# Kernel tuning notes

Measured on AMD Instinct MI355X. Metric: run time of the kernel, lower is better.

Reference implementation:

```python
import jax, jax.numpy as jnp
import numpy as np

NEG = -1e9
TAU = 1.0
N_SAMPLES = 5
SWEEP = (0.1, 0.5, 5)


def layer_norm(x, g, b, eps=1e-5):
    m = x.mean(-1, keepdims=True)
    v = x.var(-1, keepdims=True)
    return (x - m) / jnp.sqrt(v + eps) * g + b


def entmax15(z):
    # exact 1.5-entmax along last axis (Peters & Martins 2019 sort-based algorithm)
    z = z / 2.0
    zs = jnp.sort(z, axis=-1)[..., ::-1]               # descending
    T = z.shape[-1]
    kk = jnp.arange(1, T + 1, dtype=z.dtype)
    mean = jnp.cumsum(zs, -1) / kk
    mean_sq = jnp.cumsum(zs * zs, -1) / kk
    ss = kk * (mean_sq - mean * mean)
    delta = jnp.clip((1.0 - ss) / kk, 0.0)
    tau = mean - jnp.sqrt(delta)
    support = jnp.sum((tau <= zs).astype(jnp.int32), -1, keepdims=True)  # k_star
    tau_star = jnp.take_along_axis(tau, support - 1, axis=-1)
    return jnp.square(jnp.clip(z - tau_star, 0.0))


def stochastic_topk(key, scores, attn, k, tau, n_samples):
    # vectorized over samples AND batch rows with per-row variable k:
    # threshold = k-th largest perturbed score per row (ties measure-zero w/ gumbel)
    u = jax.random.uniform(key, (n_samples,) + scores.shape)
    noise = -jnp.log(-jnp.log(u + 1e-6) + 1e-6)
    pert = jnp.where(attn[None] == 0, NEG, scores[None] + noise * tau)  # [S,B,T]
    srt = jnp.sort(pert, -1)[..., ::-1]
    idx = jnp.broadcast_to((k - 1)[None, :, None], pert.shape[:2] + (1,))
    thr = jnp.take_along_axis(srt, idx, axis=-1)       # [S,B,1]
    h = (pert >= thr).astype(scores.dtype)
    return h.mean(0)                                   # [B,T]


def pool(tok, attn):
    # masked mean pooling (stand-in for sent_encoder.pool)
    return (tok * attn[..., None]).sum(1) / jnp.clip(attn.sum(1, keepdims=True), 1e-6)


def _forward(ids, embeddings, attn, ln_g, ln_b, W1, b1, W2, b2, emb_table):
    emb = embeddings * attn[..., None]
    h = jax.nn.gelu(layer_norm(emb, ln_g, ln_b) @ W1 + b1, approximate=False)
    scores = (h @ W2 + b2)[..., 0]                     # [B,T]
    scores = jnp.where(attn == 0, NEG, scores)

    tok = emb_table[ids]                               # stand-in token embeddings
    full_rep = jax.lax.stop_gradient(pool(tok, attn))  # torch.no_grad path

    T_eff = attn.sum(1)                                # [B]
    # g_soft is identical across the rho sweep in the original; hoisted here
    g_soft = entmax15(scores / TAU) * attn
    g_soft = g_soft / jnp.clip(g_soft.sum(1, keepdims=True), 1e-6)

    key = jax.random.key(42)
    rhos = np.linspace(*SWEEP)
    g_sweep, loss_sweep, rho_eff_sweep = [], [], []
    recon_sum = jnp.zeros((), embeddings.dtype)
    g = None
    for j, rho in enumerate(rhos):
        k = jnp.maximum((float(rho) * T_eff).astype(jnp.int32), 1)
        g_hard = stochastic_topk(jax.random.fold_in(key, j), scores, attn, k, TAU, N_SAMPLES)
        # straight-through: hard forward, soft (entmax) backward
        g = jax.lax.stop_gradient(g_hard) - jax.lax.stop_gradient(g_soft) + g_soft
        rho_eff_sweep.append(g.sum(1) / T_eff)
        eff_attn = attn * g
        pred_rep = pool(tok, eff_attn)
        l_r = jnp.mean(jnp.square(pred_rep - full_rep))  # recon_loss = MSE stand-in
        recon_sum = recon_sum + l_r
        g_sweep.append(g)
        loss_sweep.append(l_r)
    recon_avg = recon_sum / len(rhos)
    return g, jnp.stack(g_sweep), recon_avg, jnp.stack(loss_sweep), jnp.stack(rho_eff_sweep)


def setup_inputs() -> dict:
    key = jax.random.key(0)
    B, T, D, H, V = 8, 2048, 1024, 1365, 32000
    ks = jax.random.split(key, 8)
    return {
        "ids": jax.random.randint(ks[0], (B, T), 0, V),
        "embeddings": jax.random.normal(ks[1], (B, T, D), jnp.float32),
        "attn": jnp.ones((B, T), jnp.float32),
        "ln_g": jnp.ones((D,), jnp.float32),
        "ln_b": jnp.zeros((D,), jnp.float32),
        "W1": jax.random.normal(ks[2], (D, H), jnp.float32) * 0.02,
        "b1": jnp.zeros((H,), jnp.float32),
        "W2": jax.random.normal(ks[3], (H, 1), jnp.float32) * 0.02,
        "b2": jnp.zeros((1,), jnp.float32),
        "emb_table": jax.random.normal(ks[4], (V, D), jnp.float32) * 0.02,
    }


def reference(ids, embeddings, attn, ln_g, ln_b, W1, b1, W2, b2, emb_table):
    return _forward(ids, embeddings, attn, ln_g, ln_b, W1, b1, W2, b2, emb_table)
```

## Files before the change

### kernel.cpp

```cpp
#include <hip/hip_runtime.h>
#include <math.h>
#include <stdint.h>

#define B_ 8
#define T_ 2048
#define D_ 1024
#define H_ 1365
#define HPAD 1536
#define NTOK (B_*T_)
#define NSAMP 5
#define NRHO 5

typedef float  f32x4  __attribute__((ext_vector_type(4)));
typedef __bf16 bf16x8 __attribute__((ext_vector_type(8)));

#define WS_SCORES 0
#define WS_CNT    (WS_SCORES + NTOK*8)
#define WS_PREDW  (WS_CNT + NRHO*B_*T_*4)
#define WS_FULLW  (WS_PREDW + NRHO*B_*D_*8)
#define WS_SUMEFF (WS_FULLW + B_*D_*8)
#define WS_SUMATT (WS_SUMEFF + NRHO*B_*8)
#define WS_SUMG   (WS_SUMATT + B_*8)
#define WS_LR     (WS_SUMG + NRHO*B_*8)
#define WS_ZERO_BYTES (WS_LR + NRHO*8)
#define WS_STATS  WS_ZERO_BYTES
#define WS_W1THI  (WS_STATS + NTOK*8)
#define WS_W1TLO  (WS_W1THI + (size_t)HPAD*D_*2)
#define WS_AHI    (WS_W1TLO + (size_t)HPAD*D_*2)
#define WS_ALO    (WS_AHI + (size_t)NTOK*D_*2)
#define WS_FULL_END (WS_ALO + (size_t)NTOK*D_*2)

#define OUT_G      0
#define OUT_GSW    16384
#define OUT_RECON  98304
#define OUT_LOSS   98305
#define OUT_RHOEFF 98310

__device__ inline unsigned short f2bf(float x) {
    uint32_t u = __float_as_uint(x);
    return (unsigned short)((u + 0x7FFFu + ((u >> 16) & 1u)) >> 16);
}

__launch_bounds__(256)
__global__ void k_w1t(const float* __restrict__ W1, unsigned short* __restrict__ hi,
                      unsigned short* __restrict__ lo)
{
    __shared__ float tile[32][33];
    const int tid = threadIdx.x;
    const int bk = blockIdx.x & 31;
    const int bh = blockIdx.x >> 5;
    const int k0 = bk * 32, h0 = bh * 32;
    const int a = tid & 31, b = tid >> 5;
    #pragma unroll
    for (int i = 0; i < 4; ++i) {
        int k = k0 + b + i * 8;
        int h = h0 + a;
        tile[b + i*8][a] = (h < H_) ? W1[(size_t)k * H_ + h] : 0.0f;
    }
    __syncthreads();
    #pragma unroll
    for (int i = 0; i < 4; ++i) {
        int hrow = h0 + b + i * 8;
        int kcol = k0 + a;
        float v = tile[a][b + i*8];
        unsigned short hb = f2bf(v);
        float hf = __uint_as_float((uint32_t)hb << 16);
        unsigned short lb = f2bf(v - hf);
        size_t dst = (size_t)hrow * D_ + kcol;
        hi[dst] = hb; lo[dst] = lb;
    }
}

__launch_bounds__(256)
__global__ void k_asplit(const float* __restrict__ emb, const float* __restrict__ attn,
                         const float* __restrict__ ln_g, const float* __restrict__ ln_b,
                         unsigned short* __restrict__ ahi, unsigned short* __restrict__ alo)
{
    const int tid = threadIdx.x, l = tid & 63, w = tid >> 6;
    const int t0 = blockIdx.x * 64;
    for (int tk = w; tk < 64; tk += 4) {
        const int tg = t0 + tk;
        const float av = attn[tg];
        const float* row = emb + (size_t)tg * D_;
        float rv[16];
        double s1 = 0.0, s2 = 0.0;
        #pragma unroll
        for (int i = 0; i < 16; ++i) {
            rv[i] = row[i*64 + l];
            double x = (double)rv[i] * (double)av;
            s1 += x; s2 += x * x;
        }
        for (int m = 32; m; m >>= 1) { s1 += __shfl_xor(s1, m); s2 += __shfl_xor(s2, m); }
        double mean = s1 / (double)D_;
        double var  = s2 / (double)D_ - mean * mean;
        double inv  = 1.0 / sqrt(var + 1e-5);
        float sc  = (float)((double)av * inv);
        float nsh = -(float)(mean * inv);
        #pragma unroll
        for (int i = 0; i < 16; ++i) {
            int k = i * 64 + l;
            float t  = fmaf(rv[i], sc, nsh);
            float xn = fmaf(t, ln_g[k], ln_b[k]);
            unsigned short hb = f2bf(xn);
            float hf = __uint_as_float((uint32_t)hb << 16);
            size_t dst = (size_t)tg * D_ + k;
            ahi[dst] = hb;
            alo[dst] = f2bf(xn - hf);
        }
    }
}

__launch_bounds__(256)
__global__ void k_stats(const float* __restrict__ emb, const float* __restrict__ attn,
                        float2* __restrict__ stats)
{
    const int tid = threadIdx.x, l = tid & 63, w = tid >> 6;
    const int t0 = blockIdx.x * 64;
    for (int tk = w; tk < 64; tk += 4) {
        const int tg = t0 + tk;
        const float av = attn[tg];
        const float* row = emb + (size_t)tg * D_;
        double s1 = 0.0, s2 = 0.0;
        #pragma unroll
        for (int i = 0; i < D_/64; ++i) {
            double x = (double)row[i*64 + l] * (double)av;
            s1 += x; s2 += x * x;
        }
        for (int m = 32; m; m >>= 1) { s1 += __shfl_xor(s1, m); s2 += __shfl_xor(s2, m); }
        if (l == 0) {
            double mean = s1 / (double)D_;
            double var  = s2 / (double)D_ - mean * mean;
            double inv  = 1.0 / sqrt(var + 1e-5);
            stats[tg] = make_float2((float)((double)av * inv), (float)(mean * inv));
        }
    }
}

#define ABUF_U 8192
#define KSTEPS 32

__device__ __forceinline__ void gll16(const unsigned short* g, unsigned short* l)
{
    __builtin_amdgcn_global_load_lds((const __attribute__((address_space(1))) void*)g,
                                     (__attribute__((address_space(3))) void*)l, 16, 0, 0);
}

__launch_bounds__(512, 2)
__global__ void k_scores8(const unsigned short* __restrict__ ahi,
                          const unsigned short* __restrict__ alo,
                          const unsigned short* __restrict__ w1thi,
                          const unsigned short* __restrict__ w1tlo,
                          const float* __restrict__ b1, const float* __restrict__ W2,
                          double* __restrict__ scores)
{
    __shared__ __align__(16) unsigned short smem[3*ABUF_U];

    const int tid = threadIdx.x;
    const int blk = blockIdx.x;
    const int lin = (blk & 7) * 96 + (blk >> 3);
    const int hh = lin >> 7, mm = lin & 127;
    const int t0 = mm * 128;
    const int h0 = hh * 256;

    const int l  = tid & 63, w = tid >> 6;
    const int wr = w >> 2, wcn = w & 3;
    const int lm = l & 15, lq = l >> 4;

    const int lrow  = l >> 2;
    const int lslot = (l & 3) ^ ((l >> 3) & 3);
    const unsigned short* sA_hi = ahi + (size_t)(t0 + w*16 + lrow) * D_ + lslot*8;
    const unsigned short* sA_lo = alo + (size_t)(t0 + w*16 + lrow) * D_ + lslot*8;
    const int dA = w*512;

    const int sw8 = (lq ^ ((lm >> 1) & 3)) * 8;
    int offA[4];
    #pragma unroll
    for (int r = 0; r < 4; ++r) offA[r] = (wr*64 + r*16 + lm)*32 + sw8;

    const unsigned short* bBh = w1thi + (size_t)(h0 + wcn*64 + lm) * D_ + lq*8;
    const unsigned short* bBl = w1tlo + (size_t)(h0 + wcn*64 + lm) * D_ + lq*8;

    f32x4 acc[4][4];
    #pragma unroll
    for (int r = 0; r < 4; ++r)
        #pragma unroll
        for (int c = 0; c < 4; ++c) acc[r][c] = (f32x4){0.f, 0.f, 0.f, 0.f};

    bf16x8 bhp[2][4], blp[2][4];
    gll16(sA_hi,      &smem[0*ABUF_U + dA]);
    gll16(sA_lo,      &smem[0*ABUF_U + dA + 4096]);
    gll16(sA_hi + 32, &smem[1*ABUF_U + dA]);
    gll16(sA_lo + 32, &smem[1*ABUF_U + dA + 4096]);
    #pragma unroll
    for (int c = 0; c < 4; ++c) {
        bhp[0][c] = *(const bf16x8*)&bBh[(size_t)c*16*D_];
        blp[0][c] = *(const bf16x8*)&bBl[(size_t)c*16*D_];
    }
    #pragma unroll
    for (int c = 0; c < 4; ++c) {
        bhp[1][c] = *(const bf16x8*)&bBh[(size_t)c*16*D_ + 32];
        blp[1][c] = *(const bf16x8*)&bBl[(size_t)c*16*D_ + 32];
    }
    asm volatile("s_waitcnt vmcnt(8)" ::: "memory");
    asm volatile("s_barrier" ::: "memory");

    #pragma unroll
    for (int t = 0; t < KSTEPS; ++t) {
        const int cur = t & 1;
        bf16x8 ah[4], al[4];
        const int ab = (t % 3) * ABUF_U;
        #pragma unroll
        for (int r = 0; r < 4; ++r) ah[r] = *(const bf16x8*)&smem[ab + offA[r]];
        #pragma unroll
        for (int r = 0; r < 4; ++r) al[r] = *(const bf16x8*)&smem[ab + 4096 + offA[r]];
        if (t + 2 < KSTEPS) {
            const int ab2 = ((t + 2) % 3) * ABUF_U;
            gll16(sA_hi + (t+2)*32, &smem[ab2 + dA]);
            gll16(sA_lo + (t+2)*32, &smem[ab2 + dA + 4096]);
        }
        __builtin_amdgcn_s_setprio(1);
        #pragma unroll
        for (int r = 0; r < 4; ++r)
            #pragma unroll
            for (int c = 0; c < 4; ++c)
                acc[r][c] = __builtin_amdgcn_mfma_f32_16x16x32_bf16(ah[r], bhp[cur][c], acc[r][c], 0, 0, 0);
        #pragma unroll
        for (int r = 0; r < 4; ++r)
            #pragma unroll
            for (int c = 0; c < 4; ++c)
                acc[r][c] = __builtin_amdgcn_mfma_f32_16x16x32_bf16(ah[r], blp[cur][c], acc[r][c], 0, 0, 0);
        #pragma unroll
        for (int r = 0; r < 4; ++r)
            #pragma unroll
            for (int c = 0; c < 4; ++c)
                acc[r][c] = __builtin_amdgcn_mfma_f32_16x16x32_bf16(al[r], bhp[cur][c], acc[r][c], 0, 0, 0);
        __builtin_amdgcn_s_setprio(0);
        if (t + 2 < KSTEPS) {
            #pragma unroll
            for (int c = 0; c < 4; ++c) {
                bhp[cur][c] = *(const bf16x8*)&bBh[(size_t)c*16*D_ + (t+2)*32];
                blp[cur][c] = *(const bf16x8*)&bBl[(size_t)c*16*D_ + (t+2)*32];
            }
        }
        if (t < KSTEPS - 2)       asm volatile("s_waitcnt vmcnt(10)" ::: "memory");
        else if (t == KSTEPS - 2) asm volatile("s_waitcnt vmcnt(0)" ::: "memory");
        if (t < KSTEPS - 1)       asm volatile("s_barrier" ::: "memory");
    }

    float b1v[4], w2v[4];
    #pragma unroll
    for (int c = 0; c < 4; ++c) {
        int hg = h0 + wcn*64 + c*16 + lm;
        bool ok = (hg < H_);
        b1v[c] = ok ? b1[hg] : 0.0f;
        w2v[c] = ok ? W2[hg] : 0.0f;
    }
    const float is2 = 0.70710678118654752440f;
    #pragma unroll
    for (int r = 0; r < 4; ++r) {
        #pragma unroll
        for (int i = 0; i < 4; ++i) {
            float ps = 0.0f;
            #pragma unroll
            for (int c = 0; c < 4; ++c) {
                float z  = acc[r][c][i] + b1v[c];
                float gl = 0.5f * z * (1.0f + erff(z * is2));
                ps = fmaf(gl, w2v[c], ps);
            }
            double psd = (double)ps;
            psd += __shfl_xor(psd, 1);
            psd += __shfl_xor(psd, 2);
            psd += __shfl_xor(psd, 4);
            psd += __shfl_xor(psd, 8);
            if (lm == 0)
                atomicAdd(&scores[t0 + wr*64 + r*16 + lq*4 + i], psd);
        }
    }
}

__launch_bounds__(256)
__global__ void k_scores_fb(const float* __restrict__ emb, const float* __restrict__ ln_g,
                            const float* __restrict__ ln_b, const float2* __restrict__ stats,
                            const unsigned short* __restrict__ w1thi,
                            const unsigned short* __restrict__ w1tlo,
                            const float* __restrict__ b1, const float* __restrict__ W2,
                            double* __restrict__ scores)
{
    __shared__ __align__(16) unsigned short sAhi[128*40];
    __shared__ __align__(16) unsigned short sAlo[128*40];
    __shared__ __align__(16) unsigned short sBhi[128*40];
    __shared__ __align__(16) unsigned short sBlo[128*40];
    __shared__ float sS1[128], sS2[128];

    const int tid = threadIdx.x;
    const int blk = blockIdx.x;
    const int xcd = blk & 7, slot = blk >> 3;
    const int lin = xcd * 176 + slot;
    const int tt = lin / 11, hh = lin - tt * 11;
    const int t0 = tt * 128;
    const int h0 = hh * 128;

    if (tid < 128) {
        float2 st = stats[t0 + tid];
        sS1[tid] = st.x; sS2[tid] = st.y;
    }
    f32x4 acc[4][4];
    #pragma unroll
    for (int r = 0; r < 4; ++r)
        #pragma unroll
        for (int c = 0; c < 4; ++c) acc[r][c] = (f32x4){0.f, 0.f, 0.f, 0.f};
    const int l = tid & 63, w = tid >> 6;
    const int lm = l & 15, lq = l >> 4;
    const int wr = (w >> 1) * 64;
    const int wc = (w & 1) * 64;
    __syncthreads();

    for (int kc = 0; kc < D_; kc += 32) {
        #pragma unroll
        for (int r2 = 0; r2 < 2; ++r2) {
            int g = tid + r2 * 256;
            int row = g >> 2, oct = g & 3;
            size_t src = (size_t)(h0 + row) * D_ + kc + oct * 8;
            int dst = row * 40 + oct * 8;
            *(bf16x8*)&sBhi[dst] = *(const bf16x8*)&w1thi[src];
            *(bf16x8*)&sBlo[dst] = *(const bf16x8*)&w1tlo[src];
        }
        #pragma unroll
        for (int r2 = 0; r2 < 2; ++r2) {
            int g = tid + r2 * 256;
            int tk = g >> 2, oct = g & 3;
            int tg = t0 + tk, dg = kc + oct * 8;
            const float* ep = emb + (size_t)tg * D_ + dg;
            float s1 = sS1[tk], ns2 = -sS2[tk];
            union { unsigned short s[8]; bf16x8 v; } hi, lo;
            #pragma unroll
            for (int j = 0; j < 8; ++j) {
                float t  = fmaf(ep[j], s1, ns2);
                float xn = fmaf(t, ln_g[dg + j], ln_b[dg + j]);
                unsigned short hb = f2bf(xn);
                float hf = __uint_as_float((uint32_t)hb << 16);
                hi.s[j] = hb;
                lo.s[j] = f2bf(xn - hf);
            }
            int dst = tk * 40 + oct * 8;
            *(bf16x8*)&sAhi[dst] = hi.v;
            *(bf16x8*)&sAlo[dst] = lo.v;
        }
        __syncthreads();
        bf16x8 ah[4], al[4], bh[4], bl[4];
        #pragma unroll
        for (int r = 0; r < 4; ++r) {
            int off = (wr + r * 16 + lm) * 40 + lq * 8;
            ah[r] = *(const bf16x8*)&sAhi[off];
            al[r] = *(const bf16x8*)&sAlo[off];
        }
        #pragma unroll
        for (int c = 0; c < 4; ++c) {
            int off = (wc + c * 16 + lm) * 40 + lq * 8;
            bh[c] = *(const bf16x8*)&sBhi[off];
            bl[c] = *(const bf16x8*)&sBlo[off];
        }
        #pragma unroll
        for (int r = 0; r < 4; ++r)
            #pragma unroll
            for (int c = 0; c < 4; ++c) {
                acc[r][c] = __builtin_amdgcn_mfma_f32_16x16x32_bf16(ah[r], bh[c], acc[r][c], 0, 0, 0);
                acc[r][c] = __builtin_amdgcn_mfma_f32_16x16x32_bf16(ah[r], bl[c], acc[r][c], 0, 0, 0);
                acc[r][c] = __builtin_amdgcn_mfma_f32_16x16x32_bf16(al[r], bh[c], acc[r][c], 0, 0, 0);
            }
        __syncthreads();
    }
    float b1v[4], w2v[4];
    #pragma unroll
    for (int c = 0; c < 4; ++c) {
        int hg = h0 + wc + c * 16 + lm;
        bool ok = (hg < H_);
        b1v[c] = ok ? b1[hg] : 0.0f;
        w2v[c] = ok ? W2[hg] : 0.0f;
    }
    const float is2 = 0.70710678118654752440f;
    #pragma unroll
    for (int r = 0; r < 4; ++r) {
        #pragma unroll
        for (int i = 0; i < 4; ++i) {
            float ps = 0.0f;
            #pragma unroll
            for (int c = 0; c < 4; ++c) {
                float z  = acc[r][c][i] + b1v[c];
                float gl = 0.5f * z * (1.0f + erff(z * is2));
                ps = fmaf(gl, w2v[c], ps);
            }
            double psd = (double)ps;
            psd += __shfl_xor(psd, 1);
            psd += __shfl_xor(psd, 2);
            psd += __shfl_xor(psd, 4);
            psd += __shfl_xor(psd, 8);
            if (lm == 0)
                atomicAdd(&scores[t0 + wr + r * 16 + lq * 4 + i], psd);
        }
    }
}

__device__ inline void tf2x32(uint32_t k0, uint32_t k1, uint32_t x0, uint32_t x1,
                              uint32_t& o0, uint32_t& o1)
{
    const uint32_t ks2 = k0 ^ k1 ^ 0x1BD11BDAu;
    x0 += k0; x1 += k1;
#define ROT_(v,d) (((v) << (d)) | ((v) >> (32 - (d))))
#define RND_(R) { x0 += x1; x1 = ROT_(x1, R); x1 ^= x0; }
    RND_(13) RND_(15) RND_(26) RND_(6)
    x0 += k1;  x1 += ks2 + 1u;
    RND_(17) RND_(29) RND_(16) RND_(24)
    x0 += ks2; x1 += k0 + 2u;
    RND_(13) RND_(15) RND_(26) RND_(6)
    x0 += k0;  x1 += k1 + 3u;
    RND_(17) RND_(29) RND_(16) RND_(24)
    x0 += k1;  x1 += ks2 + 4u;
    RND_(13) RND_(15) RND_(26) RND_(6)
    x0 += ks2; x1 += k0 + 5u;
    o0 = x0; o1 = x1;
#undef RND_
#undef ROT_
}

__launch_bounds__(256)
__global__ void k_topk(const double* __restrict__ scores, const float* __restrict__ attn,
                       const float* __restrict__ b2, int* __restrict__ cnt)
{
    __shared__ unsigned long long keys[2048];
    __shared__ unsigned int hist[256];
    __shared__ unsigned int wsum[4];
    __shared__ unsigned int selDigit, selBase;
    __shared__ double red[4];

    const int tid = threadIdx.x;
    const int blk = blockIdx.x;
    const int j = blk / 40;
    const int s = (blk % 40) >> 3;
    const int b = blk & 7;

    uint32_t kk0, kk1;
    tf2x32(0u, 42u, 0u, (uint32_t)j, kk0, kk1);

    double tsum = 0.0;
    for (int t = tid; t < T_; t += 256) tsum += (double)attn[b * T_ + t];
    for (int m = 32; m; m >>= 1) tsum += __shfl_xor(tsum, m);
    if ((tid & 63) == 0) red[tid >> 6] = tsum;
    __syncthreads();
    const double Teff = red[0] + red[1] + red[2] + red[3];
    const float rhos[5] = {0.1f, 0.2f, 0.3f, 0.4f, 0.5f};
    int kst = (int)(rhos[j] * (float)Teff);
    if (kst < 1) kst = 1;

    const double bb2 = (double)b2[0];
    #pragma unroll
    for (int r = 0; r < 8; ++r) {
        int t = tid + r * 256;
        int f = (s * 8 + b) * T_ + t;
        uint32_t o0, o1;
        tf2x32(kk0, kk1, 0u, (uint32_t)f, o0, o1);
        uint32_t bits = o0 ^ o1;
        float u = __uint_as_float((bits >> 9) | 0x3f800000u) - 1.0f;
        float a1 = (float)((double)u + (double)1e-6f);
        float la = (float)log((double)a1);
        float m1 = (float)((double)1e-6f - (double)la);
        float lb = (float)log((double)m1);
        float noise = -lb;
        float av = attn[b * T_ + t];
        double pv = (av == 0.0f) ? -1e9 : (scores[b * T_ + t] + bb2 + (double)noise);
        unsigned long long uu = (unsigned long long)__double_as_longlong(pv);
        keys[t] = (uu >> 63) ? ~uu : (uu | 0x8000000000000000ull);
    }
    __syncthreads();

    unsigned long long pfx = 0;
    unsigned int plo = (unsigned int)(2048 - kst);
    const int lane = tid & 63, wv = tid >> 6;
    for (int pass = 0; pass < 8; ++pass) {
        const int shift = 56 - 8 * pass;
        const unsigned long long maskhi = (pass == 0) ? 0ull : (~0ull << (64 - 8 * pass));
        hist[tid] = 0;
        __syncthreads();
        #pragma unroll
        for (int r = 0; r < 8; ++r) {
            unsigned long long kk = keys[tid + r * 256];
            if ((kk & maskhi) == pfx)
                atomicAdd(&hist[(unsigned int)((kk >> shift) & 255ull)], 1u);
        }
        __syncthreads();
        unsigned int own = hist[tid];
        int val = (int)own;
        #pragma unroll
        for (int off = 1; off < 64; off <<= 1) {
            int n = __shfl_up(val, off);
            if (lane >= off) val += n;
        }
        if (lane == 63) wsum[wv] = (unsigned int)val;
        __syncthreads();
        unsigned int woff = 0;
        for (int q = 0; q < wv; ++q) woff += wsum[q];
        unsigned int incl = (unsigned int)val + woff;
        unsigned int excl = incl - own;
        if (own > 0 && plo >= excl && plo < incl) { selDigit = (unsigned int)tid; selBase = excl; }
        __syncthreads();
        pfx |= ((unsigned long long)selDigit << shift);
        plo -= selBase;
        __syncthreads();
    }

    #pragma unroll
    for (int r = 0; r < 8; ++r) {
        int t = tid + r * 256;
        if (keys[t] >= pfx) atomicAdd(&cnt[(j * 8 + b) * T_ + t], 1);
    }
}

__launch_bounds__(256)
__global__ void k_gfin(const int* __restrict__ cnt, const float* __restrict__ attn,
                       float* __restrict__ out, double* __restrict__ sumeff,
                       double* __restrict__ sumatt, double* __restrict__ sumg)
{
    __shared__ double redA[4], redB[4], redC[4];
    const int j = blockIdx.x >> 3, b = blockIdx.x & 7;
    const int tid = threadIdx.x;
    double sg = 0.0, se = 0.0, sa = 0.0;
    for (int t = tid; t < T_; t += 256) {
        int c = cnt[(j * 8 + b) * T_ + t];
        float g  = (float)c / 5.0f;
        float av = attn[b * T_ + t];
        out[OUT_GSW + (j * 8 + b) * T_ + t] = g;
        if (j == 4) out[OUT_G + b * T_ + t] = g;
        sg += (double)g;
        se += (double)(av * g);
        sa += (double)av;
    }
    for (int m = 32; m; m >>= 1) { sg += __shfl_xor(sg, m); se += __shfl_xor(se, m); sa += __shfl_xor(sa, m); }
    if ((tid & 63) == 0) { redA[tid>>6] = sg; redB[tid>>6] = se; redC[tid>>6] = sa; }
    __syncthreads();
    if (tid == 0) {
        sg = redA[0]+redA[1]+redA[2]+redA[3];
        se = redB[0]+redB[1]+redB[2]+redB[3];
        sa = redC[0]+redC[1]+redC[2]+redC[3];
        sumg[j*8+b] = sg; sumeff[j*8+b] = se;
        if (j == 0) sumatt[b] = sa;
        out[OUT_RHOEFF + j*8 + b] = (float)sg / (float)sa;
    }
}

__launch_bounds__(256)
__global__ void k_pool(const int* __restrict__ ids, const float* __restrict__ attn,
                       const float* __restrict__ out, const float* __restrict__ emb_table,
                       double* __restrict__ predw, double* __restrict__ fullw)
{
    __shared__ int   sid[128];
    __shared__ float sw[6][128];
    const int blk = blockIdx.x;
    const int b  = blk >> 6;
    const int dc = (blk >> 4) & 3;
    const int tc = blk & 15;
    const int tid = threadIdx.x;
    const int d = dc * 256 + tid;
    if (tid < 128) {
        int t = tc * 128 + tid;
        sid[tid] = ids[b * T_ + t];
        float av = attn[b * T_ + t];
        sw[0][tid] = av;
        #pragma unroll
        for (int j = 0; j < 5; ++j) {
            float g = out[OUT_GSW + (j * 8 + b) * T_ + t];
            sw[1 + j][tid] = av * g;
        }
    }
    __syncthreads();
    double acc[6] = {0,0,0,0,0,0};
    #pragma unroll 4
    for (int i = 0; i < 128; ++i) {
        float val = emb_table[(size_t)sid[i] * D_ + d];
        #pragma unroll
        for (int c = 0; c < 6; ++c) acc[c] += (double)(val * sw[c][i]);
    }
    atomicAdd(&fullw[b * D_ + d], acc[0]);
    #pragma unroll
    for (int j = 0; j < 5; ++j)
        atomicAdd(&predw[(j * 8 + b) * D_ + d], acc[1 + j]);
}

__launch_bounds__(256)
__global__ void k_loss(const double* __restrict__ predw, const double* __restrict__ fullw,
                       const double* __restrict__ sumeff, const double* __restrict__ sumatt,
                       float* __restrict__ out, double* __restrict__ lrws)
{
    __shared__ double red[4];
    const int j = blockIdx.x;
    const int tid = threadIdx.x;
    double p = 0.0;
    for (int i = tid; i < B_ * D_; i += 256) {
        int b = i >> 10;
        double dF = sumatt[b];        if (dF < 1e-6) dF = 1e-6;
        double dE = sumeff[j*8 + b];  if (dE < 1e-6) dE = 1e-6;
        double diff = predw[j * B_ * D_ + i] / dE - fullw[i] / dF;
        p += diff * diff;
    }
    for (int m = 32; m; m >>= 1) p += __shfl_xor(p, m);
    if ((tid & 63) == 0) red[tid >> 6] = p;
    __syncthreads();
    if (tid == 0) {
        double t = red[0] + red[1] + red[2] + red[3];
        float lr = (float)(t / (double)(B_ * D_));
        out[OUT_LOSS + j] = lr;
        lrws[j] = (double)lr;
    }
}

__launch_bounds__(64)
__global__ void k_lfin(const double* __restrict__ lrws, float* __restrict__ out)
{
    if (threadIdx.x == 0) {
        float srec = 0.0f;
        for (int j = 0; j < 5; ++j) srec += (float)lrws[j];
        out[OUT_RECON] = srec / 5.0f;
    }
}

extern "C" void kernel_launch(void* const* d_in, const int* in_sizes, int n_in,
                              void* d_out, int out_size, void* d_ws, size_t ws_size,
                              hipStream_t stream)
{
    const int*   ids  = (const int*)  d_in[0];
    const float* emb  = (const float*)d_in[1];
    const float* attn = (const float*)d_in[2];
    const float* ln_g = (const float*)d_in[3];
    const float* ln_b = (const float*)d_in[4];
    const float* W1   = (const float*)d_in[5];
    const float* b1   = (const float*)d_in[6];
    const float* W2   = (const float*)d_in[7];
    const float* b2   = (const float*)d_in[8];
    const float* et   = (const float*)d_in[9];
    float* out = (float*)d_out;
    char*  ws  = (char*)d_ws;

    double* scores = (double*)(ws + WS_SCORES);
    int*    cnt    = (int*)   (ws + WS_CNT);
    double* predw  = (double*)(ws + WS_PREDW);
    double* fullw  = (double*)(ws + WS_FULLW);
    double* sumeff = (double*)(ws + WS_SUMEFF);
    double* sumatt = (double*)(ws + WS_SUMATT);
    double* sumg   = (double*)(ws + WS_SUMG);
    double* lrws   = (double*)(ws + WS_LR);
    float2* stats  = (float2*)(ws + WS_STATS);
    unsigned short* w1thi = (unsigned short*)(ws + WS_W1THI);
    unsigned short* w1tlo = (unsigned short*)(ws + WS_W1TLO);
    unsigned short* ahi   = (unsigned short*)(ws + WS_AHI);
    unsigned short* alo   = (unsigned short*)(ws + WS_ALO);

    hipMemsetAsync(d_ws, 0, WS_ZERO_BYTES, stream);

    k_w1t<<<48*32, 256, 0, stream>>>(W1, w1thi, w1tlo);
    if (ws_size >= WS_FULL_END) {
        k_asplit<<<NTOK/64, 256, 0, stream>>>(emb, attn, ln_g, ln_b, ahi, alo);
        k_scores8<<<768, 512, 0, stream>>>(ahi, alo, w1thi, w1tlo, b1, W2, scores);
    } else {
        k_stats<<<NTOK/64, 256, 0, stream>>>(emb, attn, stats);
        k_scores_fb<<<1408, 256, 0, stream>>>(emb, ln_g, ln_b, stats, w1thi, w1tlo,
                                              b1, W2, scores);
    }
    k_topk<<<NRHO * NSAMP * B_, 256, 0, stream>>>(scores, attn, b2, cnt);
    k_gfin<<<NRHO * B_, 256, 0, stream>>>(cnt, attn, out, sumeff, sumatt, sumg);
    k_pool<<<512, 256, 0, stream>>>(ids, attn, out, et, predw, fullw);
    k_loss<<<NRHO, 256, 0, stream>>>(predw, fullw, sumeff, sumatt, out, lrws);
    k_lfin<<<1, 64, 0, stream>>>(lrws, out);
}
```

Before: 575.6 us.

## Stage W1 tiles through LDS and prefetch LDS fragments one step ahead

The B operand (W1 hi/lo transposed) is now loaded into LDS with global_load_lds alongside A, instead of each wave reading it directly from global memory into registers. A/B fragments for the next k-step are read from LDS into registers while the current step's MFMAs run, and the block-to-tile mapping changes so that consecutive blocks share a token tile across the six H tiles. The goal is to cut redundant global traffic for W1 and improve L2 reuse of A. In exchange LDS use triples to 144KB per block, which likely limits occupancy to one block per CU despite the launch bounds of two, and each step now waits on vmcnt(0) before its barrier.

```diff
diff --git a/kernel.cpp b/kernel.cpp
--- a/kernel.cpp
+++ b/kernel.cpp
@@ -136,7 +136,7 @@
     }
 }
 
-#define ABUF_U 8192
+#define BUF_U 24576
 #define KSTEPS 32
 
 __device__ __forceinline__ void gll16(const unsigned short* g, unsigned short* l)
@@ -153,12 +153,12 @@
                           const float* __restrict__ b1, const float* __restrict__ W2,
                           double* __restrict__ scores)
 {
-    __shared__ __align__(16) unsigned short smem[3*ABUF_U];
+    __shared__ __align__(16) unsigned short smem[3*BUF_U];
 
     const int tid = threadIdx.x;
     const int blk = blockIdx.x;
     const int lin = (blk & 7) * 96 + (blk >> 3);
-    const int hh = lin >> 7, mm = lin & 127;
+    const int mm = lin / 6, hh = lin - mm * 6;
     const int t0 = mm * 128;
     const int h0 = hh * 256;
 
@@ -168,17 +168,22 @@
 
     const int lrow  = l >> 2;
     const int lslot = (l & 3) ^ ((l >> 3) & 3);
-    const unsigned short* sA_hi = ahi + (size_t)(t0 + w*16 + lrow) * D_ + lslot*8;
-    const unsigned short* sA_lo = alo + (size_t)(t0 + w*16 + lrow) * D_ + lslot*8;
-    const int dA = w*512;
+    const unsigned short* sA_hi  = ahi   + (size_t)(t0 + w*16 + lrow) * D_ + lslot*8;
+    const unsigned short* sA_lo  = alo   + (size_t)(t0 + w*16 + lrow) * D_ + lslot*8;
+    const unsigned short* sB_hi0 = w1thi + (size_t)(h0 + w*32 + lrow) * D_ + lslot*8;
+    const unsigned short* sB_hi1 = sB_hi0 + 16*D_;
+    const unsigned short* sB_lo0 = w1tlo + (size_t)(h0 + w*32 + lrow) * D_ + lslot*8;
+    const unsigned short* sB_lo1 = sB_lo0 + 16*D_;
+    const int dAhi  = w*512,           dAlo  = 4096 + w*512;
+    const int dBhi0 = 8192 + w*1024,   dBhi1 = dBhi0 + 512;
+    const int dBlo0 = 16384 + w*1024,  dBlo1 = dBlo0 + 512;
 
     const int sw8 = (lq ^ ((lm >> 1) & 3)) * 8;
-    int offA[4];
+    int offA[4], offB[4];
     #pragma unroll
     for (int r = 0; r < 4; ++r) offA[r] = (wr*64 + r*16 + lm)*32 + sw8;
-
-    const unsigned short* bBh = w1thi + (size_t)(h0 + wcn*64 + lm) * D_ + lq*8;
-    const unsigned short* bBl = w1tlo + (size_t)(h0 + wcn*64 + lm) * D_ + lq*8;
+    #pragma unroll
+    for (int c = 0; c < 4; ++c) offB[c] = 8192 + (wcn*64 + c*16 + lm)*32 + sw8;
 
     f32x4 acc[4][4];
     #pragma unroll
@@ -186,65 +191,76 @@
         #pragma unroll
         for (int c = 0; c < 4; ++c) acc[r][c] = (f32x4){0.f, 0.f, 0.f, 0.f};
 
-    bf16x8 bhp[2][4], blp[2][4];
-    gll16(sA_hi,      &smem[0*ABUF_U + dA]);
-    gll16(sA_lo,      &smem[0*ABUF_U + dA + 4096]);
-    gll16(sA_hi + 32, &smem[1*ABUF_U + dA]);
-    gll16(sA_lo + 32, &smem[1*ABUF_U + dA + 4096]);
-    #pragma unroll
-    for (int c = 0; c < 4; ++c) {
-        bhp[0][c] = *(const bf16x8*)&bBh[(size_t)c*16*D_];
-        blp[0][c] = *(const bf16x8*)&bBl[(size_t)c*16*D_];
-    }
-    #pragma unroll
-    for (int c = 0; c < 4; ++c) {
-        bhp[1][c] = *(const bf16x8*)&bBh[(size_t)c*16*D_ + 32];
-        blp[1][c] = *(const bf16x8*)&bBl[(size_t)c*16*D_ + 32];
-    }
-    asm volatile("s_waitcnt vmcnt(8)" ::: "memory");
+    gll16(sA_hi,       &smem[0*BUF_U + dAhi]);
+    gll16(sA_lo,       &smem[0*BUF_U + dAlo]);
+    gll16(sB_hi0,      &smem[0*BUF_U + dBhi0]);
+    gll16(sB_hi1,      &smem[0*BUF_U + dBhi1]);
+    gll16(sB_lo0,      &smem[0*BUF_U + dBlo0]);
+    gll16(sB_lo1,      &smem[0*BUF_U + dBlo1]);
+    gll16(sA_hi  + 32, &smem[1*BUF_U + dAhi]);
+    gll16(sA_lo  + 32, &smem[1*BUF_U + dAlo]);
+    gll16(sB_hi0 + 32, &smem[1*BUF_U + dBhi0]);
+    gll16(sB_hi1 + 32, &smem[1*BUF_U + dBhi1]);
+    gll16(sB_lo0 + 32, &smem[1*BUF_U + dBlo0]);
+    gll16(sB_lo1 + 32, &smem[1*BUF_U + dBlo1]);
+    asm volatile("s_waitcnt vmcnt(6)" ::: "memory");
     asm volatile("s_barrier" ::: "memory");
 
+    bf16x8 ahp[2][4], alp[2][4], bhp[2][4];
+    #pragma unroll
+    for (int r = 0; r < 4; ++r) {
+        ahp[0][r] = *(const bf16x8*)&smem[offA[r]];
+        alp[0][r] = *(const bf16x8*)&smem[offA[r] + 4096];
+    }
+    #pragma unroll
+    for (int c = 0; c < 4; ++c) bhp[0][c] = *(const bf16x8*)&smem[offB[c]];
+
     #pragma unroll
     for (int t = 0; t < KSTEPS; ++t) {
-        const int cur = t & 1;
-        bf16x8 ah[4], al[4];
-        const int ab = (t % 3) * ABUF_U;
-        #pragma unroll
-        for (int r = 0; r < 4; ++r) ah[r] = *(const bf16x8*)&smem[ab + offA[r]];
-        #pragma unroll
-        for (int r = 0; r < 4; ++r) al[r] = *(const bf16x8*)&smem[ab + 4096 + offA[r]];
+        const int cur = t & 1, nxt = cur ^ 1;
+        asm volatile("s_waitcnt vmcnt(0)" ::: "memory");
+        asm volatile("s_barrier" ::: "memory");
         if (t + 2 < KSTEPS) {
-            const int ab2 = ((t + 2) % 3) * ABUF_U;
-            gll16(sA_hi + (t+2)*32, &smem[ab2 + dA]);
-            gll16(sA_lo + (t+2)*32, &smem[ab2 + dA + 4096]);
+            const int eb = ((t + 2) % 3) * BUF_U;
+            const int ko = (t + 2) * 32;
+            gll16(sA_hi  + ko, &smem[eb + dAhi]);
+            gll16(sA_lo  + ko, &smem[eb + dAlo]);
+            gll16(sB_hi0 + ko, &smem[eb + dBhi0]);
+            gll16(sB_hi1 + ko, &smem[eb + dBhi1]);
+            gll16(sB_lo0 + ko, &smem[eb + dBlo0]);
+            gll16(sB_lo1 + ko, &smem[eb + dBlo1]);
+        }
+        bf16x8 bl[4];
+        const int db = (t % 3) * BUF_U;
+        #pragma unroll
+        for (int c = 0; c < 4; ++c) bl[c] = *(const bf16x8*)&smem[db + offB[c] + 8192];
+        if (t + 1 < KSTEPS) {
+            const int nb = ((t + 1) % 3) * BUF_U;
+            #pragma unroll
+            for (int r = 0; r < 4; ++r) {
+                ahp[nxt][r] = *(const bf16x8*)&smem[nb + offA[r]];
+                alp[nxt][r] = *(const bf16x8*)&smem[nb + offA[r] + 4096];
+            }
+            #pragma unroll
+            for (int c = 0; c < 4; ++c) bhp[nxt][c] = *(const bf16x8*)&smem[nb + offB[c]];
         }
         __builtin_amdgcn_s_setprio(1);
         #pragma unroll
         for (int r = 0; r < 4; ++r)
             #pragma unroll
             for (int c = 0; c < 4; ++c)
-                acc[r][c] = __builtin_amdgcn_mfma_f32_16x16x32_bf16(ah[r], bhp[cur][c], acc[r][c], 0, 0, 0);
+                acc[r][c] = __builtin_amdgcn_mfma_f32_16x16x32_bf16(ahp[cur][r], bhp[cur][c], acc[r][c], 0, 0, 0);
         #pragma unroll
         for (int r = 0; r < 4; ++r)
             #pragma unroll
             for (int c = 0; c < 4; ++c)
-                acc[r][c] = __builtin_amdgcn_mfma_f32_16x16x32_bf16(ah[r], blp[cur][c], acc[r][c], 0, 0, 0);
+                acc[r][c] = __builtin_amdgcn_mfma_f32_16x16x32_bf16(ahp[cur][r], bl[c], acc[r][c], 0, 0, 0);
         #pragma unroll
         for (int r = 0; r < 4; ++r)
             #pragma unroll
             for (int c = 0; c < 4; ++c)
-                acc[r][c] = __builtin_amdgcn_mfma_f32_16x16x32_bf16(al[r], bhp[cur][c], acc[r][c], 0, 0, 0);
+                acc[r][c] = __builtin_amdgcn_mfma_f32_16x16x32_bf16(alp[cur][r], bhp[cur][c], acc[r][c], 0, 0, 0);
         __builtin_amdgcn_s_setprio(0);
-        if (t + 2 < KSTEPS) {
-            #pragma unroll
-            for (int c = 0; c < 4; ++c) {
-                bhp[cur][c] = *(const bf16x8*)&bBh[(size_t)c*16*D_ + (t+2)*32];
-                blp[cur][c] = *(const bf16x8*)&bBl[(size_t)c*16*D_ + (t+2)*32];
-            }
-        }
-        if (t < KSTEPS - 2)       asm volatile("s_waitcnt vmcnt(10)" ::: "memory");
-        else if (t == KSTEPS - 2) asm volatile("s_waitcnt vmcnt(0)" ::: "memory");
-        if (t < KSTEPS - 1)       asm volatile("s_barrier" ::: "memory");
     }
 
     float b1v[4], w2v[4];
```

Result: faster. 483.8 us (-16.0%).

## Stage both W1 and A tiles through LDS with smaller 128x128 blocks

Applied to the files above, without the earlier changes.

The scores GEMM moves from 512-thread blocks with 128x256 tiles, where W1 fragments were loaded straight from global memory into registers, to 256-thread blocks with 128x128 tiles. Both the A and W1 hi/lo operands now go through double-buffered LDS and are shared across the block's waves. The grid doubles to 1536 blocks, which trades per-wave redundant global B loads for more A re-reads across column tiles. The pipeline also drops from three stages to two, with a full vmcnt(0) wait before the barrier on every k-step, so less load latency is hidden.

```diff
diff --git a/kernel.cpp b/kernel.cpp
--- a/kernel.cpp
+++ b/kernel.cpp
@@ -136,7 +136,7 @@
     }
 }
 
-#define ABUF_U 8192
+#define BUF2_U 16384
 #define KSTEPS 32
 
 __device__ __forceinline__ void gll16(const unsigned short* g, unsigned short* l)
@@ -145,7 +145,7 @@
                                      (__attribute__((address_space(3))) void*)l, 16, 0, 0);
 }
 
-__launch_bounds__(512, 2)
+__launch_bounds__(256, 2)
 __global__ void k_scores8(const unsigned short* __restrict__ ahi,
                           const unsigned short* __restrict__ alo,
                           const unsigned short* __restrict__ w1thi,
@@ -153,32 +153,33 @@
                           const float* __restrict__ b1, const float* __restrict__ W2,
                           double* __restrict__ scores)
 {
-    __shared__ __align__(16) unsigned short smem[3*ABUF_U];
+    __shared__ __align__(16) unsigned short smem[2*BUF2_U];
 
     const int tid = threadIdx.x;
     const int blk = blockIdx.x;
-    const int lin = (blk & 7) * 96 + (blk >> 3);
-    const int hh = lin >> 7, mm = lin & 127;
+    const int lin = (blk & 7) * 192 + (blk >> 3);
+    const int mm = lin / 12, hh = lin - mm * 12;
     const int t0 = mm * 128;
-    const int h0 = hh * 256;
+    const int h0 = hh * 128;
 
     const int l  = tid & 63, w = tid >> 6;
-    const int wr = w >> 2, wcn = w & 3;
+    const int wr = w >> 1, wcn = w & 1;
     const int lm = l & 15, lq = l >> 4;
 
     const int lrow  = l >> 2;
     const int lslot = (l & 3) ^ ((l >> 3) & 3);
-    const unsigned short* sA_hi = ahi + (size_t)(t0 + w*16 + lrow) * D_ + lslot*8;
-    const unsigned short* sA_lo = alo + (size_t)(t0 + w*16 + lrow) * D_ + lslot*8;
-    const int dA = w*512;
+    const unsigned short* sA_hi = ahi   + (size_t)(t0 + w*32 + lrow) * D_ + lslot*8;
+    const unsigned short* sA_lo = alo   + (size_t)(t0 + w*32 + lrow) * D_ + lslot*8;
+    const unsigned short* sB_hi = w1thi + (size_t)(h0 + w*32 + lrow) * D_ + lslot*8;
+    const unsigned short* sB_lo = w1tlo + (size_t)(h0 + w*32 + lrow) * D_ + lslot*8;
+    const int dA = w * 1024;
 
     const int sw8 = (lq ^ ((lm >> 1) & 3)) * 8;
-    int offA[4];
+    int offA[4], offB[4];
     #pragma unroll
     for (int r = 0; r < 4; ++r) offA[r] = (wr*64 + r*16 + lm)*32 + sw8;
-
-    const unsigned short* bBh = w1thi + (size_t)(h0 + wcn*64 + lm) * D_ + lq*8;
-    const unsigned short* bBl = w1tlo + (size_t)(h0 + wcn*64 + lm) * D_ + lq*8;
+    #pragma unroll
+    for (int c = 0; c < 4; ++c) offB[c] = 8192 + (wcn*64 + c*16 + lm)*32 + sw8;
 
     f32x4 acc[4][4];
     #pragma unroll
@@ -186,65 +187,64 @@
         #pragma unroll
         for (int c = 0; c < 4; ++c) acc[r][c] = (f32x4){0.f, 0.f, 0.f, 0.f};
 
-    bf16x8 bhp[2][4], blp[2][4];
-    gll16(sA_hi,      &smem[0*ABUF_U + dA]);
-    gll16(sA_lo,      &smem[0*ABUF_U + dA + 4096]);
-    gll16(sA_hi + 32, &smem[1*ABUF_U + dA]);
-    gll16(sA_lo + 32, &smem[1*ABUF_U + dA + 4096]);
-    #pragma unroll
-    for (int c = 0; c < 4; ++c) {
-        bhp[0][c] = *(const bf16x8*)&bBh[(size_t)c*16*D_];
-        blp[0][c] = *(const bf16x8*)&bBl[(size_t)c*16*D_];
-    }
-    #pragma unroll
-    for (int c = 0; c < 4; ++c) {
-        bhp[1][c] = *(const bf16x8*)&bBh[(size_t)c*16*D_ + 32];
-        blp[1][c] = *(const bf16x8*)&bBl[(size_t)c*16*D_ + 32];
-    }
-    asm volatile("s_waitcnt vmcnt(8)" ::: "memory");
+    gll16(sA_hi,          &smem[dA]);
+    gll16(sA_hi + 16*D_,  &smem[dA + 512]);
+    gll16(sA_lo,          &smem[4096 + dA]);
+    gll16(sA_lo + 16*D_,  &smem[4096 + dA + 512]);
+    gll16(sB_hi,          &smem[8192 + dA]);
+    gll16(sB_hi + 16*D_,  &smem[8192 + dA + 512]);
+    gll16(sB_lo,          &smem[12288 + dA]);
+    gll16(sB_lo + 16*D_,  &smem[12288 + dA + 512]);
+    asm volatile("s_waitcnt vmcnt(0)" ::: "memory");
     asm volatile("s_barrier" ::: "memory");
 
     #pragma unroll
     for (int t = 0; t < KSTEPS; ++t) {
-        const int cur = t & 1;
-        bf16x8 ah[4], al[4];
-        const int ab = (t % 3) * ABUF_U;
-        #pragma unroll
-        for (int r = 0; r < 4; ++r) ah[r] = *(const bf16x8*)&smem[ab + offA[r]];
-        #pragma unroll
-        for (int r = 0; r < 4; ++r) al[r] = *(const bf16x8*)&smem[ab + 4096 + offA[r]];
-        if (t + 2 < KSTEPS) {
-            const int ab2 = ((t + 2) % 3) * ABUF_U;
-            gll16(sA_hi + (t+2)*32, &smem[ab2 + dA]);
-            gll16(sA_lo + (t+2)*32, &smem[ab2 + dA + 4096]);
+        const int db = (t & 1) * BUF2_U;
+        const int eb = db ^ BUF2_U;
+        if (t + 1 < KSTEPS) {
+            const int ko = (t + 1) * 32;
+            gll16(sA_hi + ko,         &smem[eb + dA]);
+            gll16(sA_hi + 16*D_ + ko, &smem[eb + dA + 512]);
+            gll16(sA_lo + ko,         &smem[eb + 4096 + dA]);
+            gll16(sA_lo + 16*D_ + ko, &smem[eb + 4096 + dA + 512]);
+            gll16(sB_hi + ko,         &smem[eb + 8192 + dA]);
+            gll16(sB_hi + 16*D_ + ko, &smem[eb + 8192 + dA + 512]);
+            gll16(sB_lo + ko,         &smem[eb + 12288 + dA]);
+            gll16(sB_lo + 16*D_ + ko, &smem[eb + 12288 + dA + 512]);
+        }
+        bf16x8 ah[4], al[4], bh[4], bl[4];
+        #pragma unroll
+        for (int r = 0; r < 4; ++r) {
+            ah[r] = *(const bf16x8*)&smem[db + offA[r]];
+            al[r] = *(const bf16x8*)&smem[db + offA[r] + 4096];
+        }
+        #pragma unroll
+        for (int c = 0; c < 4; ++c) {
+            bh[c] = *(const bf16x8*)&smem[db + offB[c]];
+            bl[c] = *(const bf16x8*)&smem[db + offB[c] + 4096];
         }
         __builtin_amdgcn_s_setprio(1);
         #pragma unroll
         for (int r = 0; r < 4; ++r)
             #pragma unroll
             for (int c = 0; c < 4; ++c)
-                acc[r][c] = __builtin_amdgcn_mfma_f32_16x16x32_bf16(ah[r], bhp[cur][c], acc[r][c], 0, 0, 0);
+                acc[r][c] = __builtin_amdgcn_mfma_f32_16x16x32_bf16(ah[r], bh[c], acc[r][c], 0, 0, 0);
         #pragma unroll
         for (int r = 0; r < 4; ++r)
             #pragma unroll
             for (int c = 0; c < 4; ++c)
-                acc[r][c] = __builtin_amdgcn_mfma_f32_16x16x32_bf16(ah[r], blp[cur][c], acc[r][c], 0, 0, 0);
+                acc[r][c] = __builtin_amdgcn_mfma_f32_16x16x32_bf16(ah[r], bl[c], acc[r][c], 0, 0, 0);
         #pragma unroll
         for (int r = 0; r < 4; ++r)
             #pragma unroll
             for (int c = 0; c < 4; ++c)
-                acc[r][c] = __builtin_amdgcn_mfma_f32_16x16x32_bf16(al[r], bhp[cur][c], acc[r][c], 0, 0, 0);
+                acc[r][c] = __builtin_amdgcn_mfma_f32_16x16x32_bf16(al[r], bh[c], acc[r][c], 0, 0, 0);
         __builtin_amdgcn_s_setprio(0);
-        if (t + 2 < KSTEPS) {
-            #pragma unroll
-            for (int c = 0; c < 4; ++c) {
-                bhp[cur][c] = *(const bf16x8*)&bBh[(size_t)c*16*D_ + (t+2)*32];
-                blp[cur][c] = *(const bf16x8*)&bBl[(size_t)c*16*D_ + (t+2)*32];
-            }
-        }
-        if (t < KSTEPS - 2)       asm volatile("s_waitcnt vmcnt(10)" ::: "memory");
-        else if (t == KSTEPS - 2) asm volatile("s_waitcnt vmcnt(0)" ::: "memory");
-        if (t < KSTEPS - 1)       asm volatile("s_barrier" ::: "memory");
+        if (t + 1 < KSTEPS) {
+            asm volatile("s_waitcnt vmcnt(0)" ::: "memory");
+            asm volatile("s_barrier" ::: "memory");
+        }
     }
 
     float b1v[4], w2v[4];
@@ -658,7 +658,7 @@
     k_w1t<<<48*32, 256, 0, stream>>>(W1, w1thi, w1tlo);
     if (ws_size >= WS_FULL_END) {
         k_asplit<<<NTOK/64, 256, 0, stream>>>(emb, attn, ln_g, ln_b, ahi, alo);
-        k_scores8<<<768, 512, 0, stream>>>(ahi, alo, w1thi, w1tlo, b1, W2, scores);
+        k_scores8<<<1536, 256, 0, stream>>>(ahi, alo, w1thi, w1tlo, b1, W2, scores);
     } else {
         k_stats<<<NTOK/64, 256, 0, stream>>>(emb, attn, stats);
         k_scores_fb<<<1408, 256, 0, stream>>>(emb, ln_g, ln_b, stats, w1thi, w1tlo,
```

New measurement: 490.4 us. 14.8% less time.
